# Kernel tuning notes

Measured on AMD Instinct MI355X. Metric: run time of the kernel, lower is better.

Reference implementation:

```python
import jax, jax.numpy as jnp
import numpy as np

EMBED_DIM = 768
NUM_HEADS = 12
HEAD_DIM = EMBED_DIM // NUM_HEADS


def setup_inputs() -> dict:
    key = jax.random.key(0)
    ks = jax.random.split(key, 9)
    B, N, C = 4, 2048, EMBED_DIM
    s = 1.0 / np.sqrt(C)
    x = jax.random.normal(ks[0], (B, N, C), dtype=jnp.float32)
    Wq = jax.random.normal(ks[1], (C, C), dtype=jnp.float32) * s
    bq = jnp.zeros((C,), dtype=jnp.float32)
    Wk = jax.random.normal(ks[2], (C, C), dtype=jnp.float32) * s
    bk = jnp.zeros((C,), dtype=jnp.float32)
    Wv = jax.random.normal(ks[3], (C, C), dtype=jnp.float32) * s
    bv = jnp.zeros((C,), dtype=jnp.float32)
    Wo = jax.random.normal(ks[4], (C, C), dtype=jnp.float32) * s
    bo = jnp.zeros((C,), dtype=jnp.float32)
    return {"x": x, "Wq": Wq, "bq": bq, "Wk": Wk, "bk": bk,
            "Wv": Wv, "bv": bv, "Wo": Wo, "bo": bo}


def reference(x, Wq, bq, Wk, bk, Wv, bv, Wo, bo):
    # Dropout in eval mode (identity), matching module.eval().
    B, N, C = x.shape
    H, D = NUM_HEADS, HEAD_DIM
    scale = D ** -0.5

    def split_heads(t):  # [B,N,C] -> [B,H,N,D]
        return t.reshape(B, N, H, D).transpose(0, 2, 1, 3)

    q = split_heads(x @ Wq.T + bq)
    k = split_heads(x @ Wk.T + bk)
    v = split_heads(x @ Wv.T + bv)

    attn = jnp.einsum('bhnd,bhmd->bhnm', q, k) * scale  # [B,H,N,N]
    attn = jax.nn.softmax(attn, axis=-1)
    out = jnp.einsum('bhnm,bhmd->bhnd', attn, v)        # [B,H,N,D]
    out = out.transpose(0, 2, 1, 3).reshape(B, N, C)
    return out @ Wo.T + bo
```

## Files before the change

### kernel.cpp

```cpp
#include <hip/hip_runtime.h>
#include <math.h>

#define CDIM 768
#define NHEADS 12
#define HDIM 64
#define BATCH 4
#define SEQ 2048
#define MTOT (BATCH*SEQ)
#define NQKV (3*CDIM)
#define QROWS 128
#define VTILE 4096

typedef __attribute__((ext_vector_type(8))) short bf16x8;
typedef __attribute__((ext_vector_type(4))) short bf16x4;
typedef __attribute__((ext_vector_type(4))) float f32x4;
typedef unsigned short u16;
typedef unsigned int u32;

#define ASYNC16(gsrc, ldst) \
  __builtin_amdgcn_global_load_lds((const __attribute__((address_space(1))) void*)(gsrc), \
                                   (__attribute__((address_space(3))) void*)(ldst), 16, 0, 0)

__device__ inline u16 f2b(float x) {
    unsigned int u = __float_as_uint(x);
    return (u16)((u + 0x7fffu + ((u >> 16) & 1u)) >> 16);
}
__device__ inline u32 prnd(float x) { return __float_as_uint(x) + 0x8000u; }

#define XBLK (MTOT*CDIM/1024)
#define WBLK (CDIM*CDIM/1024)
__global__ __launch_bounds__(256)
void prep_kern(const float* __restrict__ x,
               const float* __restrict__ Wq, const float* __restrict__ Wk,
               const float* __restrict__ Wv, const float* __restrict__ Wo,
               const float* __restrict__ bq, const float* __restrict__ bk,
               const float* __restrict__ bv,
               u16* __restrict__ xb, u16* __restrict__ wqkv, u16* __restrict__ wob,
               float* __restrict__ bcat)
{
    int bx = blockIdx.x, tid = threadIdx.x;
    if (bx < XBLK) {
        int i = (bx * 256 + tid) * 4;
        float4 v = *(const float4*)(x + i);
        ushort4 o;
        o.x = f2b(v.x); o.y = f2b(v.y); o.z = f2b(v.z); o.w = f2b(v.w);
        *(ushort4*)(xb + i) = o;
    } else if (bx < XBLK + 4*WBLK) {
        int z = (bx - XBLK) / WBLK;
        int blk = (bx - XBLK) % WBLK;
        const float* src = (z == 0) ? Wq : (z == 1) ? Wk : (z == 2) ? Wv : Wo;
        u16* dst = (z == 3) ? wob : wqkv + (size_t)z * CDIM * CDIM;
        int i = (blk * 256 + tid) * 4;
        float4 v = *(const float4*)(src + i);
        ushort4 o;
        o.x = f2b(v.x); o.y = f2b(v.y); o.z = f2b(v.z); o.w = f2b(v.w);
        *(ushort4*)(dst + i) = o;
    } else {
        int i = (bx - XBLK - 4*WBLK) * 256 + tid;
        if (i < CDIM) bcat[i] = bq[i];
        else if (i < 2*CDIM) bcat[i] = bk[i - CDIM];
        else if (i < 3*CDIM) bcat[i] = bv[i - 2*CDIM];
    }
}

template<int OUTF32>
__global__ __launch_bounds__(256)
void gemm_bf16(const u16* __restrict__ A, const u16* __restrict__ B,
               const float* __restrict__ bias, void* __restrict__ Y,
               int N, int K, int qn, float qscale)
{
    __shared__ __align__(16) u16 As[128*64];
    __shared__ __align__(16) u16 Bs[128*64];
    const int tid = threadIdx.x;
    const int m0 = blockIdx.y * 128, n0 = blockIdx.x * 128;
    const int wid = tid >> 6, lane = tid & 63;
    const int wm = (wid & 1) * 64, wn = (wid >> 1) * 64;
    const int l15 = lane & 15, quad = lane >> 4;

    f32x4 acc[4][4];
    #pragma unroll
    for (int i = 0; i < 4; ++i)
        #pragma unroll
        for (int j = 0; j < 4; ++j)
            #pragma unroll
            for (int r = 0; r < 4; ++r) acc[i][j][r] = 0.f;

    for (int k0 = 0; k0 < K; k0 += 64) {
        __syncthreads();
        #pragma unroll
        for (int r = 0; r < 4; ++r) {
            int li = r*256 + tid;
            int row = li >> 3, c = li & 7;
            int gc = c ^ (row & 7);
            ASYNC16(A + (size_t)(m0 + row) * K + k0 + gc*8, &As[li*8]);
            ASYNC16(B + (size_t)(n0 + row) * K + k0 + gc*8, &Bs[li*8]);
        }
        __syncthreads();
        #pragma unroll
        for (int kk = 0; kk < 2; ++kk) {
            bf16x8 a[4], b[4];
            #pragma unroll
            for (int i = 0; i < 4; ++i) {
                int m = wm + i*16 + l15;
                int ca = (kk*4 + quad) ^ (m & 7);
                a[i] = *(const bf16x8*)&As[m*64 + ca*8];
                int n = wn + i*16 + l15;
                int cb = (kk*4 + quad) ^ (n & 7);
                b[i] = *(const bf16x8*)&Bs[n*64 + cb*8];
            }
            #pragma unroll
            for (int i = 0; i < 4; ++i)
                #pragma unroll
                for (int j = 0; j < 4; ++j)
                    acc[i][j] = __builtin_amdgcn_mfma_f32_16x16x32_bf16(a[i], b[j], acc[i][j], 0, 0, 0);
        }
    }

    #pragma unroll
    for (int i = 0; i < 4; ++i) {
        #pragma unroll
        for (int j = 0; j < 4; ++j) {
            int gn = n0 + wn + j*16 + l15;
            float bv = bias[gn];
            float sc = (gn < qn) ? qscale : 1.0f;
            #pragma unroll
            for (int r = 0; r < 4; ++r) {
                int gm = m0 + wm + i*16 + quad*4 + r;
                float v = (acc[i][j][r] + bv) * sc;
                if (OUTF32) ((float*)Y)[(size_t)gm * N + gn] = v;
                else        ((u16*)Y)[(size_t)gm * N + gn] = f2b(v);
            }
        }
    }
}

__global__ __launch_bounds__(256)
void transpose_v(const u16* __restrict__ QKV, u16* __restrict__ Vt)
{
    __shared__ __align__(16) u16 Vs[64*72];
    const int tid = threadIdx.x;
    const int nt = blockIdx.x, bh = blockIdx.y;
    const int b = bh / NHEADS, h = bh % NHEADS;
    const u16* src = QKV + ((size_t)(b*SEQ + nt*64)) * NQKV + 2*CDIM + h*HDIM;
    #pragma unroll
    for (int rep = 0; rep < 2; ++rep) {
        int li = rep*256 + tid, r = li >> 3, c = li & 7;
        *(uint4*)&Vs[r*72 + c*8] = *(const uint4*)(src + (size_t)r * NQKV + c*8);
    }
    __syncthreads();
    u16* dst = Vt + ((size_t)bh * 32 + nt) * VTILE;
    #pragma unroll
    for (int rep = 0; rep < 2; ++rep) {
        int p = rep*256 + tid;
        int frag = p >> 5;
        int ks = frag >> 2, jd = frag & 3;
        int lane0 = (p & 31) * 2;
        int quad = lane0 >> 4, l15e = lane0 & 15;
        int d0 = jd*16 + l15e;
        int sb = ks*16 + quad*4;
        u32 r0 = *(const u32*)&Vs[(sb+0)*72 + d0];
        u32 r1 = *(const u32*)&Vs[(sb+1)*72 + d0];
        u32 r2 = *(const u32*)&Vs[(sb+2)*72 + d0];
        u32 r3 = *(const u32*)&Vs[(sb+3)*72 + d0];
        uint4 o;
        o.x = __builtin_amdgcn_perm(r1, r0, 0x05040100u);
        o.y = __builtin_amdgcn_perm(r3, r2, 0x05040100u);
        o.z = __builtin_amdgcn_perm(r1, r0, 0x07060302u);
        o.w = __builtin_amdgcn_perm(r3, r2, 0x07060302u);
        *(uint4*)(dst + (size_t)(frag*64 + lane0) * 4) = o;
    }
}

__global__ __launch_bounds__(256, 3)
void attn_mfma(const u16* __restrict__ QK, const u16* __restrict__ Vt,
               u16* __restrict__ Oa)
{
    __shared__ __align__(16) u16 Ks[2][64*64];

    const int tid = threadIdx.x;
    const int wid = tid >> 6, lane = tid & 63;
    const int l15 = lane & 15, quad = lane >> 4;
    const int qt = blockIdx.x, bh = blockIdx.y;
    const int b = bh / NHEADS, h = bh % NHEADS;

    const u16* Qg  = QK + ((size_t)(b*SEQ + qt*QROWS)) * NQKV + h*HDIM;
    const u16* Kg0 = QK + ((size_t)(b*SEQ)) * NQKV + CDIM + h*HDIM;
    const uint2* Vg = (const uint2*)(Vt + (size_t)bh * 32 * VTILE);

    #pragma unroll
    for (int r = 0; r < 2; ++r) {
        int li = r*256 + tid, row = li >> 3, c = li & 7, gc = c ^ (row & 7);
        ASYNC16(Kg0 + (size_t)row * NQKV + gc*8, &Ks[0][li*8]);
    }
    uint2 vb[2][16];
    #pragma unroll
    for (int f = 0; f < 16; ++f) vb[0][f] = Vg[f*64 + lane];

    bf16x8 qf[2][2];
    #pragma unroll
    for (int mb = 0; mb < 2; ++mb)
        #pragma unroll
        for (int kk = 0; kk < 2; ++kk)
            qf[mb][kk] = *(const bf16x8*)(Qg + (size_t)(wid*32 + mb*16 + l15) * NQKV + kk*32 + quad*8);

    const bf16x4 ONES = { (short)0x3F80, (short)0x3F80, (short)0x3F80, (short)0x3F80 };

    f32x4 o[2][4];
    #pragma unroll
    for (int mb = 0; mb < 2; ++mb)
        #pragma unroll
        for (int j = 0; j < 4; ++j)
            #pragma unroll
            for (int r = 0; r < 4; ++r) o[mb][j][r] = 0.f;
    f32x4 ll[2];
    #pragma unroll
    for (int mb = 0; mb < 2; ++mb)
        #pragma unroll
        for (int r = 0; r < 4; ++r) ll[mb][r] = 0.f;

    __syncthreads();

    auto body = [&](int kt, int cbuf, int nbuf) {
        if (kt + 1 < SEQ/64) {
            #pragma unroll
            for (int r = 0; r < 2; ++r) {
                int li = r*256 + tid, row = li >> 3, c = li & 7, gc = c ^ (row & 7);
                ASYNC16(Kg0 + (size_t)((kt+1)*64 + row) * NQKV + gc*8, &Ks[nbuf][li*8]);
            }
            const uint2* vsrc = Vg + (size_t)(kt+1) * (VTILE/4);
            #pragma unroll
            for (int f = 0; f < 16; ++f) vb[nbuf][f] = vsrc[f*64 + lane];
        }

        f32x4 s[2][4];
        #pragma unroll
        for (int mb = 0; mb < 2; ++mb)
            #pragma unroll
            for (int j = 0; j < 4; ++j)
                #pragma unroll
                for (int r = 0; r < 4; ++r) s[mb][j][r] = 0.f;
        #pragma unroll
        for (int kk = 0; kk < 2; ++kk) {
            #pragma unroll
            for (int j = 0; j < 4; ++j) {
                int kr = j*16 + l15;
                int ck = (kk*4 + quad) ^ (kr & 7);
                bf16x8 ak = *(const bf16x8*)&Ks[cbuf][kr*64 + ck*8];
                #pragma unroll
                for (int mb = 0; mb < 2; ++mb)
                    s[mb][j] = __builtin_amdgcn_mfma_f32_16x16x32_bf16(ak, qf[mb][kk], s[mb][j], 0, 0, 0);
            }
        }

        bf16x4 pf[2][4];
        #pragma unroll
        for (int mb = 0; mb < 2; ++mb)
            #pragma unroll
            for (int ks = 0; ks < 4; ++ks) {
                u32 u0 = prnd(__builtin_amdgcn_exp2f(s[mb][ks][0]));
                u32 u1 = prnd(__builtin_amdgcn_exp2f(s[mb][ks][1]));
                u32 u2 = prnd(__builtin_amdgcn_exp2f(s[mb][ks][2]));
                u32 u3 = prnd(__builtin_amdgcn_exp2f(s[mb][ks][3]));
                union { uint2 u; bf16x4 v; } cst;
                cst.u.x = __builtin_amdgcn_perm(u1, u0, 0x07060302u);
                cst.u.y = __builtin_amdgcn_perm(u3, u2, 0x07060302u);
                pf[mb][ks] = cst.v;
            }

        #pragma unroll
        for (int ks = 0; ks < 4; ++ks) {
            #pragma unroll
            for (int jd = 0; jd < 4; ++jd) {
                union { uint2 u; bf16x4 v; } vv;
                vv.u = vb[cbuf][ks*4 + jd];
                #pragma unroll
                for (int mb = 0; mb < 2; ++mb)
                    o[mb][jd] = __builtin_amdgcn_mfma_f32_16x16x16bf16_1k(pf[mb][ks], vv.v, o[mb][jd], 0, 0, 0);
            }
            #pragma unroll
            for (int mb = 0; mb < 2; ++mb)
                ll[mb] = __builtin_amdgcn_mfma_f32_16x16x16bf16_1k(pf[mb][ks], ONES, ll[mb], 0, 0, 0);
        }
        __syncthreads();
    };

    for (int kt = 0; kt < SEQ/64; kt += 2) {
        body(kt,   0, 1);
        body(kt+1, 1, 0);
    }

    u16* Og = Oa + ((size_t)(b*SEQ + qt*QROWS)) * CDIM + h*HDIM;
    #pragma unroll
    for (int mb = 0; mb < 2; ++mb) {
        #pragma unroll
        for (int r = 0; r < 4; ++r) {
            float inv = 1.f / ll[mb][r];
            int row = wid*32 + mb*16 + quad*4 + r;
            #pragma unroll
            for (int jd = 0; jd < 4; ++jd)
                Og[(size_t)row * CDIM + jd*16 + l15] = f2b(o[mb][jd][r] * inv);
        }
    }
}

extern "C" void kernel_launch(void* const* d_in, const int* in_sizes, int n_in,
                              void* d_out, int out_size, void* d_ws, size_t ws_size,
                              hipStream_t stream)
{
    const float* x  = (const float*)d_in[0];
    const float* Wq = (const float*)d_in[1];
    const float* bq = (const float*)d_in[2];
    const float* Wk = (const float*)d_in[3];
    const float* bk = (const float*)d_in[4];
    const float* Wv = (const float*)d_in[5];
    const float* bv = (const float*)d_in[6];
    const float* Wo = (const float*)d_in[7];
    const float* bo = (const float*)d_in[8];

    unsigned char* ws = (unsigned char*)d_ws;
    u16* xb   = (u16*)ws;  ws += (size_t)MTOT * CDIM * 2;
    u16* wqkv = (u16*)ws;  ws += (size_t)NQKV * CDIM * 2;
    u16* wob  = (u16*)ws;  ws += (size_t)CDIM * CDIM * 2;
    float* bcat = (float*)ws; ws += (size_t)NQKV * 4;
    u16* qkv  = (u16*)ws;  ws += (size_t)MTOT * NQKV * 2;
    u16* vt   = (u16*)ws;  ws += (size_t)BATCH*NHEADS*32*VTILE * 2;
    u16* ao   = (u16*)ws;

    prep_kern<<<XBLK + 4*WBLK + 9, 256, 0, stream>>>(x, Wq, Wk, Wv, Wo, bq, bk, bv,
                                                     xb, wqkv, wob, bcat);

    gemm_bf16<0><<<dim3(NQKV/128, MTOT/128), 256, 0, stream>>>(xb, wqkv, bcat, qkv, NQKV, CDIM, CDIM, 0.18033688f);
    transpose_v<<<dim3(SEQ/64, BATCH*NHEADS), 256, 0, stream>>>(qkv, vt);
    attn_mfma<<<dim3(SEQ/QROWS, BATCH*NHEADS), 256, 0, stream>>>(qkv, vt, ao);
    gemm_bf16<1><<<dim3(CDIM/128, MTOT/128), 256, 0, stream>>>(ao, wob, bo, (float*)d_out, CDIM, CDIM, 0, 1.0f);
}
```

Baseline: 248.7 us.

## Fuse V fragment transpose into QKV GEMM epilogue and stage V in LDS

```diff
diff --git a/kernel.cpp b/kernel.cpp
--- a/kernel.cpp
+++ b/kernel.cpp
@@ -63,10 +63,11 @@
     }
 }
 
-template<int OUTF32>
+template<int OUTF32, int VFRAG>
 __global__ __launch_bounds__(256)
 void gemm_bf16(const u16* __restrict__ A, const u16* __restrict__ B,
                const float* __restrict__ bias, void* __restrict__ Y,
+               u16* __restrict__ Vt,
                int N, int K, int qn, float qscale)
 {
     __shared__ __align__(16) u16 As[128*64];
@@ -116,58 +117,47 @@
         }
     }
 
-    #pragma unroll
-    for (int i = 0; i < 4; ++i) {
-        #pragma unroll
-        for (int j = 0; j < 4; ++j) {
-            int gn = n0 + wn + j*16 + l15;
-            float bv = bias[gn];
-            float sc = (gn < qn) ? qscale : 1.0f;
-            #pragma unroll
-            for (int r = 0; r < 4; ++r) {
-                int gm = m0 + wm + i*16 + quad*4 + r;
-                float v = (acc[i][j][r] + bv) * sc;
-                if (OUTF32) ((float*)Y)[(size_t)gm * N + gn] = v;
-                else        ((u16*)Y)[(size_t)gm * N + gn] = f2b(v);
-            }
-        }
-    }
-}
-
-__global__ __launch_bounds__(256)
-void transpose_v(const u16* __restrict__ QKV, u16* __restrict__ Vt)
-{
-    __shared__ __align__(16) u16 Vs[64*72];
-    const int tid = threadIdx.x;
-    const int nt = blockIdx.x, bh = blockIdx.y;
-    const int b = bh / NHEADS, h = bh % NHEADS;
-    const u16* src = QKV + ((size_t)(b*SEQ + nt*64)) * NQKV + 2*CDIM + h*HDIM;
-    #pragma unroll
-    for (int rep = 0; rep < 2; ++rep) {
-        int li = rep*256 + tid, r = li >> 3, c = li & 7;
-        *(uint4*)&Vs[r*72 + c*8] = *(const uint4*)(src + (size_t)r * NQKV + c*8);
-    }
-    __syncthreads();
-    u16* dst = Vt + ((size_t)bh * 32 + nt) * VTILE;
-    #pragma unroll
-    for (int rep = 0; rep < 2; ++rep) {
-        int p = rep*256 + tid;
-        int frag = p >> 5;
-        int ks = frag >> 2, jd = frag & 3;
-        int lane0 = (p & 31) * 2;
-        int quad = lane0 >> 4, l15e = lane0 & 15;
-        int d0 = jd*16 + l15e;
-        int sb = ks*16 + quad*4;
-        u32 r0 = *(const u32*)&Vs[(sb+0)*72 + d0];
-        u32 r1 = *(const u32*)&Vs[(sb+1)*72 + d0];
-        u32 r2 = *(const u32*)&Vs[(sb+2)*72 + d0];
-        u32 r3 = *(const u32*)&Vs[(sb+3)*72 + d0];
-        uint4 o;
-        o.x = __builtin_amdgcn_perm(r1, r0, 0x05040100u);
-        o.y = __builtin_amdgcn_perm(r3, r2, 0x05040100u);
-        o.z = __builtin_amdgcn_perm(r1, r0, 0x07060302u);
-        o.w = __builtin_amdgcn_perm(r3, r2, 0x07060302u);
-        *(uint4*)(dst + (size_t)(frag*64 + lane0) * 4) = o;
+    if (VFRAG && n0 >= 2*CDIM) {
+        #pragma unroll
+        for (int i = 0; i < 4; ++i) {
+            int gm = m0 + wm + i*16 + quad*4;
+            int bb = gm >> 11;
+            int kt = (gm & 2047) >> 6;
+            int ks = (gm & 63) >> 4;
+            #pragma unroll
+            for (int j = 0; j < 4; ++j) {
+                int gn = n0 + wn + j*16 + l15;
+                float bv = bias[gn];
+                int d = gn - 2*CDIM;
+                int h = d >> 6, jd = (d & 63) >> 4;
+                int bh = bb * NHEADS + h;
+                u32 p0 = prnd(acc[i][j][0] + bv);
+                u32 p1 = prnd(acc[i][j][1] + bv);
+                u32 p2 = prnd(acc[i][j][2] + bv);
+                u32 p3 = prnd(acc[i][j][3] + bv);
+                uint2 st;
+                st.x = __builtin_amdgcn_perm(p1, p0, 0x07060302u);
+                st.y = __builtin_amdgcn_perm(p3, p2, 0x07060302u);
+                *(uint2*)(Vt + ((size_t)(bh*32 + kt))*VTILE + (size_t)((ks*4 + jd)*64 + lane)*4) = st;
+            }
+        }
+    } else {
+        #pragma unroll
+        for (int i = 0; i < 4; ++i) {
+            #pragma unroll
+            for (int j = 0; j < 4; ++j) {
+                int gn = n0 + wn + j*16 + l15;
+                float bv = bias[gn];
+                float sc = (gn < qn) ? qscale : 1.0f;
+                #pragma unroll
+                for (int r = 0; r < 4; ++r) {
+                    int gm = m0 + wm + i*16 + quad*4 + r;
+                    float v = (acc[i][j][r] + bv) * sc;
+                    if (OUTF32) ((float*)Y)[(size_t)gm * N + gn] = v;
+                    else        ((u16*)Y)[(size_t)gm * N + gn] = f2b(v);
+                }
+            }
+        }
     }
 }
 
@@ -176,6 +166,7 @@
                u16* __restrict__ Oa)
 {
     __shared__ __align__(16) u16 Ks[2][64*64];
+    __shared__ __align__(16) u16 Vls[2][VTILE];
 
     const int tid = threadIdx.x;
     const int wid = tid >> 6, lane = tid & 63;
@@ -185,16 +176,14 @@
 
     const u16* Qg  = QK + ((size_t)(b*SEQ + qt*QROWS)) * NQKV + h*HDIM;
     const u16* Kg0 = QK + ((size_t)(b*SEQ)) * NQKV + CDIM + h*HDIM;
-    const uint2* Vg = (const uint2*)(Vt + (size_t)bh * 32 * VTILE);
+    const u16* Vg  = Vt + (size_t)bh * 32 * VTILE;
 
     #pragma unroll
     for (int r = 0; r < 2; ++r) {
         int li = r*256 + tid, row = li >> 3, c = li & 7, gc = c ^ (row & 7);
         ASYNC16(Kg0 + (size_t)row * NQKV + gc*8, &Ks[0][li*8]);
-    }
-    uint2 vb[2][16];
-    #pragma unroll
-    for (int f = 0; f < 16; ++f) vb[0][f] = Vg[f*64 + lane];
+        ASYNC16(Vg + li*8, &Vls[0][li*8]);
+    }
 
     bf16x8 qf[2][2];
     #pragma unroll
@@ -226,10 +215,8 @@
             for (int r = 0; r < 2; ++r) {
                 int li = r*256 + tid, row = li >> 3, c = li & 7, gc = c ^ (row & 7);
                 ASYNC16(Kg0 + (size_t)((kt+1)*64 + row) * NQKV + gc*8, &Ks[nbuf][li*8]);
-            }
-            const uint2* vsrc = Vg + (size_t)(kt+1) * (VTILE/4);
-            #pragma unroll
-            for (int f = 0; f < 16; ++f) vb[nbuf][f] = vsrc[f*64 + lane];
+                ASYNC16(Vg + (size_t)(kt+1) * VTILE + li*8, &Vls[nbuf][li*8]);
+            }
         }
 
         f32x4 s[2][4];
@@ -271,11 +258,10 @@
         for (int ks = 0; ks < 4; ++ks) {
             #pragma unroll
             for (int jd = 0; jd < 4; ++jd) {
-                union { uint2 u; bf16x4 v; } vv;
-                vv.u = vb[cbuf][ks*4 + jd];
+                bf16x4 vv = *(const bf16x4*)&Vls[cbuf][(size_t)((ks*4 + jd)*64 + lane)*4];
                 #pragma unroll
                 for (int mb = 0; mb < 2; ++mb)
-                    o[mb][jd] = __builtin_amdgcn_mfma_f32_16x16x16bf16_1k(pf[mb][ks], vv.v, o[mb][jd], 0, 0, 0);
+                    o[mb][jd] = __builtin_amdgcn_mfma_f32_16x16x16bf16_1k(pf[mb][ks], vv, o[mb][jd], 0, 0, 0);
             }
             #pragma unroll
             for (int mb = 0; mb < 2; ++mb)
@@ -329,8 +315,7 @@
     prep_kern<<<XBLK + 4*WBLK + 9, 256, 0, stream>>>(x, Wq, Wk, Wv, Wo, bq, bk, bv,
                                                      xb, wqkv, wob, bcat);
 
-    gemm_bf16<0><<<dim3(NQKV/128, MTOT/128), 256, 0, stream>>>(xb, wqkv, bcat, qkv, NQKV, CDIM, CDIM, 0.18033688f);
-    transpose_v<<<dim3(SEQ/64, BATCH*NHEADS), 256, 0, stream>>>(qkv, vt);
+    gemm_bf16<0,1><<<dim3(NQKV/128, MTOT/128), 256, 0, stream>>>(xb, wqkv, bcat, qkv, vt, NQKV, CDIM, CDIM, 0.18033688f);
     attn_mfma<<<dim3(SEQ/QROWS, BATCH*NHEADS), 256, 0, stream>>>(qkv, vt, ao);
-    gemm_bf16<1><<<dim3(CDIM/128, MTOT/128), 256, 0, stream>>>(ao, wob, bo, (float*)d_out, CDIM, CDIM, 0, 1.0f);
-}
+    gemm_bf16<1,0><<<dim3(CDIM/128, MTOT/128), 256, 0, stream>>>(ao, wob, bo, (float*)d_out, nullptr, CDIM, CDIM, 0, 1.0f);
+}
```

Measured after the change: 227.8 us. 8.4% less time.
